# Kernel optimization log

Hardware: AMD Instinct MI355X
Metric: run time of the kernel (lower is better)

Reference implementation:

```python
import jax, jax.numpy as jnp
import numpy as np

N = 100000
E = 1600000
IN, HID, OUT = 128, 256, 128


def setup_inputs() -> dict:
    key = jax.random.key(0)
    ks = jax.random.split(key, 12)
    x = jax.random.normal(ks[0], (N, IN), dtype=jnp.float32)
    edge_index = jax.random.randint(ks[1], (2, E), 0, N, dtype=jnp.int64)
    def lin(k, fan_in, fan_out):
        bound = 1.0 / np.sqrt(fan_in)
        return jax.random.uniform(k, (fan_in, fan_out), jnp.float32, -bound, bound)
    return {
        "x": x,
        "edge_index": edge_index,
        # SAGEConv layer 1 (in -> hidden): Wl on aggregated neighbors (with bias), Wr on root
        "Wl1": lin(ks[2], IN, HID), "Wr1": lin(ks[3], IN, HID), "b1": jnp.zeros((HID,), jnp.float32),
        # SAGEConv layer 2 (hidden -> out)
        "Wl2": lin(ks[4], HID, OUT), "Wr2": lin(ks[5], HID, OUT), "b2": jnp.zeros((OUT,), jnp.float32),
        # classifier MLP: out -> hidden -> 2
        "Wc1": lin(ks[6], OUT, HID), "bc1": jnp.zeros((HID,), jnp.float32),
        "Wc2": lin(ks[7], HID, 2), "bc2": jnp.zeros((2,), jnp.float32),
    }


def _sage_conv(x, src, dst, Wl, Wr, b):
    # mean-aggregate neighbor features into dst, then lin_l(agg) + lin_r(x)
    agg = jax.ops.segment_sum(x[src], dst, num_segments=N)          # [N, d]
    cnt = jax.ops.segment_sum(jnp.ones((src.shape[0],), x.dtype), dst, num_segments=N)
    mean = agg / jnp.maximum(cnt, 1.0)[:, None]
    return mean @ Wl + x @ Wr + b


def reference(x, edge_index, Wl1, Wr1, b1, Wl2, Wr2, b2, Wc1, bc1, Wc2, bc2):
    src, dst = edge_index[0], edge_index[1]
    h = jax.nn.relu(_sage_conv(x, src, dst, Wl1, Wr1, b1))  # dropout = identity (eval)
    h = _sage_conv(h, src, dst, Wl2, Wr2, b2)               # node embeddings [N, OUT]
    logits = jax.nn.relu(h @ Wc1 + bc1) @ Wc2 + bc2          # [N, 2]
    return (h, logits)
```

## Files before the change

### kernel.cpp

```cpp
#include <hip/hip_runtime.h>

#define MAXDEG 64
#define BINSHIFT 10
#define CAP 20480
#define CHUNK 4096

typedef __bf16 bf16x8 __attribute__((ext_vector_type(8)));
typedef float f32x4 __attribute__((ext_vector_type(4)));

__device__ inline ushort f2bf(float f) {
    unsigned u = __builtin_bit_cast(unsigned, f);
    return (ushort)((u + 0x7fffu + ((u >> 16) & 1u)) >> 16);
}
__device__ inline float bf2f(ushort h) {
    unsigned u = ((unsigned)h) << 16;
    return __builtin_bit_cast(float, u);
}

__device__ inline void split8(const float* __restrict__ p, bf16x8& hi, bf16x8& lo) {
    float4 v0 = *(const float4*)p;
    float4 v1 = *(const float4*)(p + 4);
    float f[8] = {v0.x, v0.y, v0.z, v0.w, v1.x, v1.y, v1.z, v1.w};
    #pragma unroll
    for (int j = 0; j < 8; ++j) {
        __bf16 h = (__bf16)f[j];
        hi[j] = h;
        lo[j] = (__bf16)(f[j] - (float)h);
    }
}

__global__ __launch_bounds__(256) void bin_edges(
    const int* __restrict__ src, const int* __restrict__ dst,
    int* __restrict__ bincnt, uint2* __restrict__ binbuf, int E)
{
    __shared__ int hist[128];
    __shared__ int base[128];
    const int t = threadIdx.x;
    if (t < 128) hist[t] = 0;
    __syncthreads();

    const int e0 = blockIdx.x * CHUNK;
    int s[16], d[16], sl[16];
    #pragma unroll
    for (int j = 0; j < 16; ++j) {
        int e = e0 + j * 256 + t;
        if (e < E) {
            s[j]  = src[e];
            d[j]  = dst[e];
            sl[j] = atomicAdd(&hist[d[j] >> BINSHIFT], 1);
        } else {
            d[j] = -1;
        }
    }
    __syncthreads();
    if (t < 128 && hist[t] > 0) base[t] = atomicAdd(&bincnt[t], hist[t]);
    __syncthreads();
    #pragma unroll
    for (int j = 0; j < 16; ++j) {
        if (d[j] >= 0) {
            int b = d[j] >> BINSHIFT;
            int pos = base[b] + sl[j];
            if (pos < CAP)
                binbuf[(size_t)b * CAP + pos] = make_uint2((unsigned)s[j], (unsigned)d[j]);
        }
    }
}

__global__ __launch_bounds__(512) void fill_buckets(
    const int* __restrict__ bincnt, const uint2* __restrict__ binbuf,
    int* __restrict__ deg, int* __restrict__ col, int N)
{
    __shared__ int ldeg[1024];
    const int b = blockIdx.x;
    const int t = threadIdx.x;
    ldeg[t] = 0;
    ldeg[t + 512] = 0;
    __syncthreads();
    int cnt = bincnt[b];
    cnt = cnt < CAP ? cnt : CAP;
    const uint2* seg = binbuf + (size_t)b * CAP;
    for (int i = t; i < cnt; i += 512) {
        uint2 e = seg[i];
        int slot = atomicAdd(&ldeg[e.y & 1023], 1);
        if (slot < MAXDEG) col[(size_t)e.y * MAXDEG + slot] = (int)e.x;
    }
    __syncthreads();
    int nb = b << BINSHIFT;
    #pragma unroll
    for (int u = 0; u < 2; ++u) {
        int i = t + u * 512;
        int node = nb + i;
        if (node < N) deg[node] = ldeg[i];
    }
}

__global__ __launch_bounds__(256) void xtobf(
    const float* __restrict__ X, ushort* __restrict__ Xb, int n4)
{
    int i = blockIdx.x * 256 + threadIdx.x;
    if (i >= n4) return;
    float4 v = *(const float4*)(X + (size_t)i * 4);
    *(ushort4*)(Xb + (size_t)i * 4) =
        make_ushort4(f2bf(v.x), f2bf(v.y), f2bf(v.z), f2bf(v.w));
}

__global__ __launch_bounds__(256) void wsplit(
    const float* __restrict__ W, ushort* __restrict__ Thi, ushort* __restrict__ Tlo,
    int K, int N)
{
    int idx = blockIdx.x * 256 + threadIdx.x;
    if (idx >= K * N) return;
    int n = idx / K, k = idx % K;
    float v = W[(size_t)k * N + n];
    ushort h = f2bf(v);
    Thi[idx] = h;
    Tlo[idx] = f2bf(v - bf2f(h));
}

__global__ void make_bcat(const float* __restrict__ b2, float* __restrict__ bcat) {
    int t = threadIdx.x;
    bcat[t] = t < 128 ? 0.f : b2[t - 128];
}

__global__ __launch_bounds__(256) void init_logits(
    const float* __restrict__ bc2, float* __restrict__ out, int M)
{
    int n = blockIdx.x * 256 + threadIdx.x;
    if (n < M) *(float2*)(out + (size_t)n * 2) = make_float2(bc2[0], bc2[1]);
}

__global__ __launch_bounds__(256) void agg_mean_bf16(
    const ushort* __restrict__ Xb, const int* __restrict__ col,
    const int* __restrict__ deg, float* __restrict__ out, int N)
{
    int gw = (blockIdx.x * 256 + threadIdx.x) >> 6;
    if (gw >= N) return;
    int lane = threadIdx.x & 63;
    int d = deg[gw];
    int dc = d < MAXDEG ? d : MAXDEG;
    const int* cl = col + (size_t)gw * MAXDEG;
    float a0 = 0.f, a1 = 0.f;
    int i = 0;
    for (; i + 4 <= dc; i += 4) {
        int4 id4 = *(const int4*)(cl + i);
        ushort2 v0 = *(const ushort2*)(Xb + (size_t)id4.x * 128 + lane * 2);
        ushort2 v1 = *(const ushort2*)(Xb + (size_t)id4.y * 128 + lane * 2);
        ushort2 v2 = *(const ushort2*)(Xb + (size_t)id4.z * 128 + lane * 2);
        ushort2 v3 = *(const ushort2*)(Xb + (size_t)id4.w * 128 + lane * 2);
        a0 += (bf2f(v0.x) + bf2f(v1.x)) + (bf2f(v2.x) + bf2f(v3.x));
        a1 += (bf2f(v0.y) + bf2f(v1.y)) + (bf2f(v2.y) + bf2f(v3.y));
    }
    for (; i < dc; ++i) {
        ushort2 v = *(const ushort2*)(Xb + (size_t)cl[i] * 128 + lane * 2);
        a0 += bf2f(v.x); a1 += bf2f(v.y);
    }
    float inv = 1.0f / (float)(d > 1 ? d : 1);
    *(float2*)(out + (size_t)gw * 128 + lane * 2) = make_float2(a0 * inv, a1 * inv);
}

__global__ __launch_bounds__(256) void agg_finish(
    const ushort* __restrict__ t2b, const float* __restrict__ tcat2,
    const int* __restrict__ col, const int* __restrict__ deg,
    float* __restrict__ h2, int N)
{
    int gw = (blockIdx.x * 256 + threadIdx.x) >> 6;
    if (gw >= N) return;
    int lane = threadIdx.x & 63;
    int d = deg[gw];
    int dc = d < MAXDEG ? d : MAXDEG;
    const int* cl = col + (size_t)gw * MAXDEG;
    float a0 = 0.f, a1 = 0.f;
    int i = 0;
    for (; i + 4 <= dc; i += 4) {
        int4 id4 = *(const int4*)(cl + i);
        ushort2 v0 = *(const ushort2*)(t2b + (size_t)id4.x * 128 + lane * 2);
        ushort2 v1 = *(const ushort2*)(t2b + (size_t)id4.y * 128 + lane * 2);
        ushort2 v2 = *(const ushort2*)(t2b + (size_t)id4.z * 128 + lane * 2);
        ushort2 v3 = *(const ushort2*)(t2b + (size_t)id4.w * 128 + lane * 2);
        a0 += (bf2f(v0.x) + bf2f(v1.x)) + (bf2f(v2.x) + bf2f(v3.x));
        a1 += (bf2f(v0.y) + bf2f(v1.y)) + (bf2f(v2.y) + bf2f(v3.y));
    }
    for (; i < dc; ++i) {
        ushort2 v = *(const ushort2*)(t2b + (size_t)cl[i] * 128 + lane * 2);
        a0 += bf2f(v.x); a1 += bf2f(v.y);
    }
    float inv = 1.0f / (float)(d > 1 ? d : 1);
    float2 hp = *(const float2*)(tcat2 + (size_t)gw * 128 + lane * 2);
    *(float2*)(h2 + (size_t)gw * 128 + lane * 2) =
        make_float2(a0 * inv + hp.x, a1 * inv + hp.y);
}

template<int K, int NPH, int MODE>
__global__ __launch_bounds__(512, 4) void gemm_tile(
    const float* __restrict__ A1, const float* __restrict__ A2,
    const ushort* __restrict__ B1hi, const ushort* __restrict__ B1lo,
    const ushort* __restrict__ B2hi, const ushort* __restrict__ B2lo,
    const float* __restrict__ bias, const float* __restrict__ Wc2,
    float* __restrict__ outf, ushort* __restrict__ outt2, int M, int relu)
{
    __shared__ __align__(16) ushort Ah[128 * 40];
    __shared__ __align__(16) ushort Al[128 * 40];
    __shared__ __align__(16) ushort BhS[256 * 40];
    __shared__ __align__(16) ushort BlS[256 * 40];
    __shared__ float sw0[256], sw1[256];

    const int t = threadIdx.x;
    if constexpr (MODE == 1) {
        if (t < 256) {
            sw0[t] = Wc2[t * 2 + 0];
            sw1[t] = Wc2[t * 2 + 1];
        }
    }

    const int m0 = blockIdx.x * 128;
    const int l  = t & 63;
    const int wv = t >> 6;
    const int wr = (wv >> 1) * 32;
    const int wc = (wv & 1) * 128;
    const int lr = l & 15;
    const int kb = l >> 4;

    const int sra = t >> 2;
    const int sq  = t & 3;
    const int srb = t >> 1;
    const int sh  = t & 1;

    f32x4 acc[2][8] = {};

    #pragma unroll
    for (int ph = 0; ph < NPH; ++ph) {
        const float*  A  = ph ? A2 : A1;
        const ushort* Bh = ph ? B2hi : B1hi;
        const ushort* Bl = ph ? B2lo : B1lo;
        for (int k0 = 0; k0 < K; k0 += 32) {
            __syncthreads();
            {
                int rg = m0 + sra;
                rg = rg < M ? rg : M - 1;
                const float* p = A + (size_t)rg * K + k0 + sq * 8;
                bf16x8 h0, l0;
                split8(p, h0, l0);
                int base = sra * 40 + sq * 8;
                *(bf16x8*)&Ah[base] = h0;
                *(bf16x8*)&Al[base] = l0;
            }
            {
                const ushort* ph_ = Bh + (size_t)srb * K + k0 + sh * 16;
                const ushort* pl_ = Bl + (size_t)srb * K + k0 + sh * 16;
                int base = srb * 40 + sh * 16;
                *(uint4*)&BhS[base]     = *(const uint4*)ph_;
                *(uint4*)&BhS[base + 8] = *(const uint4*)(ph_ + 8);
                *(uint4*)&BlS[base]     = *(const uint4*)pl_;
                *(uint4*)&BlS[base + 8] = *(const uint4*)(pl_ + 8);
            }
            __syncthreads();
            bf16x8 ah[2], al_[2];
            #pragma unroll
            for (int mi = 0; mi < 2; ++mi) {
                int off = (wr + mi * 16 + lr) * 40 + kb * 8;
                ah[mi]  = *(const bf16x8*)&Ah[off];
                al_[mi] = *(const bf16x8*)&Al[off];
            }
            #pragma unroll
            for (int nj = 0; nj < 8; ++nj) {
                int off = (wc + nj * 16 + lr) * 40 + kb * 8;
                bf16x8 bh = *(const bf16x8*)&BhS[off];
                bf16x8 bl = *(const bf16x8*)&BlS[off];
                #pragma unroll
                for (int mi = 0; mi < 2; ++mi) {
                    acc[mi][nj] = __builtin_amdgcn_mfma_f32_16x16x32_bf16(ah[mi],  bh, acc[mi][nj], 0, 0, 0);
                    acc[mi][nj] = __builtin_amdgcn_mfma_f32_16x16x32_bf16(al_[mi], bh, acc[mi][nj], 0, 0, 0);
                    acc[mi][nj] = __builtin_amdgcn_mfma_f32_16x16x32_bf16(ah[mi],  bl, acc[mi][nj], 0, 0, 0);
                }
            }
        }
    }

    if constexpr (MODE != 1) {
        #pragma unroll
        for (int nj = 0; nj < 8; ++nj) {
            int colg = wc + nj * 16 + lr;
            float bv = bias[colg];
            #pragma unroll
            for (int mi = 0; mi < 2; ++mi) {
                #pragma unroll
                for (int reg = 0; reg < 4; ++reg) {
                    int rowg = m0 + wr + mi * 16 + kb * 4 + reg;
                    if (rowg >= M) continue;
                    float v = acc[mi][nj][reg] + bv;
                    if (relu) v = fmaxf(v, 0.f);
                    if constexpr (MODE == 0) {
                        outf[(size_t)rowg * 256 + colg] = v;
                    } else {
                        if (wc == 0) outt2[(size_t)rowg * 128 + colg] = f2bf(v);
                        else         outf[(size_t)rowg * 128 + colg - 128] = v;
                    }
                }
            }
        }
    } else {
        #pragma unroll
        for (int mi = 0; mi < 2; ++mi) {
            #pragma unroll
            for (int reg = 0; reg < 4; ++reg) {
                float s0 = 0.f, s1 = 0.f;
                #pragma unroll
                for (int nj = 0; nj < 8; ++nj) {
                    int colg = wc + nj * 16 + lr;
                    float v = fmaxf(acc[mi][nj][reg] + bias[colg], 0.f);
                    s0 += v * sw0[colg];
                    s1 += v * sw1[colg];
                }
                #pragma unroll
                for (int mk = 1; mk < 16; mk <<= 1) {
                    s0 += __shfl_xor(s0, mk);
                    s1 += __shfl_xor(s1, mk);
                }
                int rowg = m0 + wr + mi * 16 + kb * 4 + reg;
                if (lr == 0 && rowg < M) {
                    atomicAdd(&outf[(size_t)rowg * 2 + 0], s0);
                    atomicAdd(&outf[(size_t)rowg * 2 + 1], s1);
                }
            }
        }
    }
}

extern "C" void kernel_launch(void* const* d_in, const int* in_sizes, int n_in,
                              void* d_out, int out_size, void* d_ws, size_t ws_size,
                              hipStream_t stream)
{
    const float* x   = (const float*)d_in[0];
    const int*   ei  = (const int*)d_in[1];
    const float* Wl1 = (const float*)d_in[2];
    const float* Wr1 = (const float*)d_in[3];
    const float* b1  = (const float*)d_in[4];
    const float* Wl2 = (const float*)d_in[5];
    const float* Wr2 = (const float*)d_in[6];
    const float* b2  = (const float*)d_in[7];
    const float* Wc1 = (const float*)d_in[8];
    const float* bc1 = (const float*)d_in[9];
    const float* Wc2 = (const float*)d_in[10];
    const float* bc2 = (const float*)d_in[11];

    const int N = in_sizes[0] / 128;
    const int E = in_sizes[1] / 2;
    const int nbins = (N + (1 << BINSHIFT) - 1) >> BINSHIFT;

    char* ws = (char*)d_ws;
    size_t off = 0;
    auto alloc = [&](size_t bytes) -> void* {
        void* p = ws + off;
        off += (bytes + 255) & ~(size_t)255;
        return p;
    };
    const size_t NE128 = (size_t)N * 128;
    const size_t NE256 = (size_t)N * 256;

    int*    bincnt = (int*)alloc((size_t)nbins * 4);
    int*    deg  = (int*)alloc((size_t)N * 4);
    int*    colb = (int*)alloc((size_t)N * MAXDEG * 4);
    char*   bufA = (char*)alloc(NE256 * 4);
    char*   bufB = (char*)alloc(NE256 * 4);
    ushort* wl1h = (ushort*)alloc(256 * 128 * 2); ushort* wl1l = (ushort*)alloc(256 * 128 * 2);
    ushort* wr1h = (ushort*)alloc(256 * 128 * 2); ushort* wr1l = (ushort*)alloc(256 * 128 * 2);
    ushort* w2h  = (ushort*)alloc(256 * 256 * 2); ushort* w2l  = (ushort*)alloc(256 * 256 * 2);
    ushort* wc1h = (ushort*)alloc(256 * 128 * 2); ushort* wc1l = (ushort*)alloc(256 * 128 * 2);
    float*  bcat = (float*)alloc(256 * 4);

    uint2*  binbuf = (uint2*)bufA;
    float*  a1    = (float*)bufA;
    ushort* t2b   = (ushort*)bufA;
    float*  tcat2 = (float*)(bufA + NE128 * 2);
    ushort* xb    = (ushort*)bufB;
    float*  h1    = (float*)bufB;

    float* h2     = (float*)d_out;
    float* logits = (float*)d_out + NE128;

    const int gm = (N + 127) / 128;

    hipMemsetAsync(bincnt, 0, (size_t)nbins * 4, stream);

    bin_edges<<<dim3((E + CHUNK - 1) / CHUNK), dim3(256), 0, stream>>>(
        ei, ei + E, bincnt, binbuf, E);
    fill_buckets<<<dim3(nbins), dim3(512), 0, stream>>>(bincnt, binbuf, deg, colb, N);

    xtobf<<<dim3((int)(NE128 / 4 + 255) / 256), dim3(256), 0, stream>>>(x, xb, (int)(NE128 / 4));
    wsplit<<<dim3(128), dim3(256), 0, stream>>>(Wl1, wl1h, wl1l, 128, 256);
    wsplit<<<dim3(128), dim3(256), 0, stream>>>(Wr1, wr1h, wr1l, 128, 256);
    wsplit<<<dim3(128), dim3(256), 0, stream>>>(Wl2, w2h, w2l, 256, 128);
    wsplit<<<dim3(128), dim3(256), 0, stream>>>(Wr2, w2h + 128 * 256, w2l + 128 * 256, 256, 128);
    wsplit<<<dim3(128), dim3(256), 0, stream>>>(Wc1, wc1h, wc1l, 128, 256);
    make_bcat<<<dim3(1), dim3(256), 0, stream>>>(b2, bcat);
    init_logits<<<dim3((N + 255) / 256), dim3(256), 0, stream>>>(bc2, logits, N);

    agg_mean_bf16<<<dim3((N + 3) / 4), dim3(256), 0, stream>>>(xb, colb, deg, a1, N);
    gemm_tile<128, 2, 0><<<dim3(gm), dim3(512), 0, stream>>>(
        a1, x, wl1h, wl1l, wr1h, wr1l, b1, nullptr, h1, nullptr, N, 1);

    gemm_tile<256, 1, 3><<<dim3(gm), dim3(512), 0, stream>>>(
        h1, nullptr, w2h, w2l, nullptr, nullptr, bcat, nullptr, tcat2, t2b, N, 0);

    agg_finish<<<dim3((N + 3) / 4), dim3(256), 0, stream>>>(
        t2b, tcat2, colb, deg, h2, N);

    gemm_tile<128, 1, 1><<<dim3(gm), dim3(512), 0, stream>>>(
        h2, nullptr, wc1h, wc1l, nullptr, nullptr, bc1, Wc2, logits, nullptr, N, 1);
}
```

Before: 428.0 us.

## Split GEMM columns across a 2D grid and widen gather loads to 8 bytes

The GEMM kernel now tiles the output 128 columns per block with a second grid dimension, so each block does half the N-width. This halves the accumulator and LDS footprint per block, which should raise occupancy and give more blocks, but the A tile, including its hi/lo split, is now loaded and converted twice. The aggregation kernels split each 64-lane wave into two half-waves that take alternate neighbour groups with 8-byte loads, then combine through a cross-lane shuffle. That doubles the number of gathers in flight per wave.

```diff
diff --git a/kernel.cpp b/kernel.cpp
--- a/kernel.cpp
+++ b/kernel.cpp
@@ -136,26 +136,38 @@
     int gw = (blockIdx.x * 256 + threadIdx.x) >> 6;
     if (gw >= N) return;
     int lane = threadIdx.x & 63;
+    int sub = lane >> 5;
+    int c4  = (lane & 31) * 4;
     int d = deg[gw];
     int dc = d < MAXDEG ? d : MAXDEG;
     const int* cl = col + (size_t)gw * MAXDEG;
-    float a0 = 0.f, a1 = 0.f;
+    float a0 = 0.f, a1 = 0.f, a2 = 0.f, a3 = 0.f;
     int i = 0;
-    for (; i + 4 <= dc; i += 4) {
-        int4 id4 = *(const int4*)(cl + i);
-        ushort2 v0 = *(const ushort2*)(Xb + (size_t)id4.x * 128 + lane * 2);
-        ushort2 v1 = *(const ushort2*)(Xb + (size_t)id4.y * 128 + lane * 2);
-        ushort2 v2 = *(const ushort2*)(Xb + (size_t)id4.z * 128 + lane * 2);
-        ushort2 v3 = *(const ushort2*)(Xb + (size_t)id4.w * 128 + lane * 2);
+    for (; i + 8 <= dc; i += 8) {
+        int4 id = *(const int4*)(cl + i + sub * 4);
+        ushort4 v0 = *(const ushort4*)(Xb + (size_t)id.x * 128 + c4);
+        ushort4 v1 = *(const ushort4*)(Xb + (size_t)id.y * 128 + c4);
+        ushort4 v2 = *(const ushort4*)(Xb + (size_t)id.z * 128 + c4);
+        ushort4 v3 = *(const ushort4*)(Xb + (size_t)id.w * 128 + c4);
         a0 += (bf2f(v0.x) + bf2f(v1.x)) + (bf2f(v2.x) + bf2f(v3.x));
         a1 += (bf2f(v0.y) + bf2f(v1.y)) + (bf2f(v2.y) + bf2f(v3.y));
-    }
-    for (; i < dc; ++i) {
-        ushort2 v = *(const ushort2*)(Xb + (size_t)cl[i] * 128 + lane * 2);
-        a0 += bf2f(v.x); a1 += bf2f(v.y);
-    }
-    float inv = 1.0f / (float)(d > 1 ? d : 1);
-    *(float2*)(out + (size_t)gw * 128 + lane * 2) = make_float2(a0 * inv, a1 * inv);
+        a2 += (bf2f(v0.z) + bf2f(v1.z)) + (bf2f(v2.z) + bf2f(v3.z));
+        a3 += (bf2f(v0.w) + bf2f(v1.w)) + (bf2f(v2.w) + bf2f(v3.w));
+    }
+    for (; i < dc; i += 2) {
+        int j = i + sub;
+        if (j < dc) {
+            ushort4 v = *(const ushort4*)(Xb + (size_t)cl[j] * 128 + c4);
+            a0 += bf2f(v.x); a1 += bf2f(v.y); a2 += bf2f(v.z); a3 += bf2f(v.w);
+        }
+    }
+    a0 += __shfl_xor(a0, 32); a1 += __shfl_xor(a1, 32);
+    a2 += __shfl_xor(a2, 32); a3 += __shfl_xor(a3, 32);
+    if (sub == 0) {
+        float inv = 1.0f / (float)(d > 1 ? d : 1);
+        *(float4*)(out + (size_t)gw * 128 + c4) =
+            make_float4(a0 * inv, a1 * inv, a2 * inv, a3 * inv);
+    }
 }
 
 __global__ __launch_bounds__(256) void agg_finish(
@@ -166,28 +178,39 @@
     int gw = (blockIdx.x * 256 + threadIdx.x) >> 6;
     if (gw >= N) return;
     int lane = threadIdx.x & 63;
+    int sub = lane >> 5;
+    int c4  = (lane & 31) * 4;
     int d = deg[gw];
     int dc = d < MAXDEG ? d : MAXDEG;
     const int* cl = col + (size_t)gw * MAXDEG;
-    float a0 = 0.f, a1 = 0.f;
+    float a0 = 0.f, a1 = 0.f, a2 = 0.f, a3 = 0.f;
     int i = 0;
-    for (; i + 4 <= dc; i += 4) {
-        int4 id4 = *(const int4*)(cl + i);
-        ushort2 v0 = *(const ushort2*)(t2b + (size_t)id4.x * 128 + lane * 2);
-        ushort2 v1 = *(const ushort2*)(t2b + (size_t)id4.y * 128 + lane * 2);
-        ushort2 v2 = *(const ushort2*)(t2b + (size_t)id4.z * 128 + lane * 2);
-        ushort2 v3 = *(const ushort2*)(t2b + (size_t)id4.w * 128 + lane * 2);
+    for (; i + 8 <= dc; i += 8) {
+        int4 id = *(const int4*)(cl + i + sub * 4);
+        ushort4 v0 = *(const ushort4*)(t2b + (size_t)id.x * 128 + c4);
+        ushort4 v1 = *(const ushort4*)(t2b + (size_t)id.y * 128 + c4);
+        ushort4 v2 = *(const ushort4*)(t2b + (size_t)id.z * 128 + c4);
+        ushort4 v3 = *(const ushort4*)(t2b + (size_t)id.w * 128 + c4);
         a0 += (bf2f(v0.x) + bf2f(v1.x)) + (bf2f(v2.x) + bf2f(v3.x));
         a1 += (bf2f(v0.y) + bf2f(v1.y)) + (bf2f(v2.y) + bf2f(v3.y));
-    }
-    for (; i < dc; ++i) {
-        ushort2 v = *(const ushort2*)(t2b + (size_t)cl[i] * 128 + lane * 2);
-        a0 += bf2f(v.x); a1 += bf2f(v.y);
-    }
-    float inv = 1.0f / (float)(d > 1 ? d : 1);
-    float2 hp = *(const float2*)(tcat2 + (size_t)gw * 128 + lane * 2);
-    *(float2*)(h2 + (size_t)gw * 128 + lane * 2) =
-        make_float2(a0 * inv + hp.x, a1 * inv + hp.y);
+        a2 += (bf2f(v0.z) + bf2f(v1.z)) + (bf2f(v2.z) + bf2f(v3.z));
+        a3 += (bf2f(v0.w) + bf2f(v1.w)) + (bf2f(v2.w) + bf2f(v3.w));
+    }
+    for (; i < dc; i += 2) {
+        int j = i + sub;
+        if (j < dc) {
+            ushort4 v = *(const ushort4*)(t2b + (size_t)cl[j] * 128 + c4);
+            a0 += bf2f(v.x); a1 += bf2f(v.y); a2 += bf2f(v.z); a3 += bf2f(v.w);
+        }
+    }
+    a0 += __shfl_xor(a0, 32); a1 += __shfl_xor(a1, 32);
+    a2 += __shfl_xor(a2, 32); a3 += __shfl_xor(a3, 32);
+    if (sub == 0) {
+        float inv = 1.0f / (float)(d > 1 ? d : 1);
+        float4 hp = *(const float4*)(tcat2 + (size_t)gw * 128 + c4);
+        *(float4*)(h2 + (size_t)gw * 128 + c4) = make_float4(
+            a0 * inv + hp.x, a1 * inv + hp.y, a2 * inv + hp.z, a3 * inv + hp.w);
+    }
 }
 
 template<int K, int NPH, int MODE>
@@ -200,9 +223,9 @@
 {
     __shared__ __align__(16) ushort Ah[128 * 40];
     __shared__ __align__(16) ushort Al[128 * 40];
-    __shared__ __align__(16) ushort BhS[256 * 40];
-    __shared__ __align__(16) ushort BlS[256 * 40];
-    __shared__ float sw0[256], sw1[256];
+    __shared__ __align__(16) ushort BhS[128 * 40];
+    __shared__ __align__(16) ushort BlS[128 * 40];
+    __shared__ float sw0[MODE == 1 ? 256 : 4], sw1[MODE == 1 ? 256 : 4];
 
     const int t = threadIdx.x;
     if constexpr (MODE == 1) {
@@ -213,19 +236,18 @@
     }
 
     const int m0 = blockIdx.x * 128;
+    const int n0 = blockIdx.y * 128;
     const int l  = t & 63;
     const int wv = t >> 6;
     const int wr = (wv >> 1) * 32;
-    const int wc = (wv & 1) * 128;
+    const int wc = (wv & 1) * 64;
     const int lr = l & 15;
     const int kb = l >> 4;
 
-    const int sra = t >> 2;
-    const int sq  = t & 3;
-    const int srb = t >> 1;
-    const int sh  = t & 1;
-
-    f32x4 acc[2][8] = {};
+    const int sr = t >> 2;
+    const int sq = t & 3;
+
+    f32x4 acc[2][4] = {};
 
     #pragma unroll
     for (int ph = 0; ph < NPH; ++ph) {
@@ -235,23 +257,21 @@
         for (int k0 = 0; k0 < K; k0 += 32) {
             __syncthreads();
             {
-                int rg = m0 + sra;
+                int rg = m0 + sr;
                 rg = rg < M ? rg : M - 1;
                 const float* p = A + (size_t)rg * K + k0 + sq * 8;
                 bf16x8 h0, l0;
                 split8(p, h0, l0);
-                int base = sra * 40 + sq * 8;
+                int base = sr * 40 + sq * 8;
                 *(bf16x8*)&Ah[base] = h0;
                 *(bf16x8*)&Al[base] = l0;
             }
             {
-                const ushort* ph_ = Bh + (size_t)srb * K + k0 + sh * 16;
-                const ushort* pl_ = Bl + (size_t)srb * K + k0 + sh * 16;
-                int base = srb * 40 + sh * 16;
-                *(uint4*)&BhS[base]     = *(const uint4*)ph_;
-                *(uint4*)&BhS[base + 8] = *(const uint4*)(ph_ + 8);
-                *(uint4*)&BlS[base]     = *(const uint4*)pl_;
-                *(uint4*)&BlS[base + 8] = *(const uint4*)(pl_ + 8);
+                const ushort* ph_ = Bh + (size_t)(n0 + sr) * K + k0 + sq * 8;
+                const ushort* pl_ = Bl + (size_t)(n0 + sr) * K + k0 + sq * 8;
+                int base = sr * 40 + sq * 8;
+                *(uint4*)&BhS[base] = *(const uint4*)ph_;
+                *(uint4*)&BlS[base] = *(const uint4*)pl_;
             }
             __syncthreads();
             bf16x8 ah[2], al_[2];
@@ -262,7 +282,7 @@
                 al_[mi] = *(const bf16x8*)&Al[off];
             }
             #pragma unroll
-            for (int nj = 0; nj < 8; ++nj) {
+            for (int nj = 0; nj < 4; ++nj) {
                 int off = (wc + nj * 16 + lr) * 40 + kb * 8;
                 bf16x8 bh = *(const bf16x8*)&BhS[off];
                 bf16x8 bl = *(const bf16x8*)&BlS[off];
@@ -278,8 +298,9 @@
 
     if constexpr (MODE != 1) {
         #pragma unroll
-        for (int nj = 0; nj < 8; ++nj) {
-            int colg = wc + nj * 16 + lr;
+        for (int nj = 0; nj < 4; ++nj) {
+            int lc   = wc + nj * 16 + lr;
+            int colg = n0 + lc;
             float bv = bias[colg];
             #pragma unroll
             for (int mi = 0; mi < 2; ++mi) {
@@ -292,8 +313,8 @@
                     if constexpr (MODE == 0) {
                         outf[(size_t)rowg * 256 + colg] = v;
                     } else {
-                        if (wc == 0) outt2[(size_t)rowg * 128 + colg] = f2bf(v);
-                        else         outf[(size_t)rowg * 128 + colg - 128] = v;
+                        if (n0 == 0) outt2[(size_t)rowg * 128 + lc] = f2bf(v);
+                        else         outf[(size_t)rowg * 128 + lc] = v;
                     }
                 }
             }
@@ -305,8 +326,8 @@
             for (int reg = 0; reg < 4; ++reg) {
                 float s0 = 0.f, s1 = 0.f;
                 #pragma unroll
-                for (int nj = 0; nj < 8; ++nj) {
-                    int colg = wc + nj * 16 + lr;
+                for (int nj = 0; nj < 4; ++nj) {
+                    int colg = n0 + wc + nj * 16 + lr;
                     float v = fmaxf(acc[mi][nj][reg] + bias[colg], 0.f);
                     s0 += v * sw0[colg];
                     s1 += v * sw1[colg];
@@ -396,15 +417,15 @@
     init_logits<<<dim3((N + 255) / 256), dim3(256), 0, stream>>>(bc2, logits, N);
 
     agg_mean_bf16<<<dim3((N + 3) / 4), dim3(256), 0, stream>>>(xb, colb, deg, a1, N);
-    gemm_tile<128, 2, 0><<<dim3(gm), dim3(512), 0, stream>>>(
+    gemm_tile<128, 2, 0><<<dim3(gm, 2), dim3(512), 0, stream>>>(
         a1, x, wl1h, wl1l, wr1h, wr1l, b1, nullptr, h1, nullptr, N, 1);
 
-    gemm_tile<256, 1, 3><<<dim3(gm), dim3(512), 0, stream>>>(
+    gemm_tile<256, 1, 3><<<dim3(gm, 2), dim3(512), 0, stream>>>(
         h1, nullptr, w2h, w2l, nullptr, nullptr, bcat, nullptr, tcat2, t2b, N, 0);
 
     agg_finish<<<dim3((N + 3) / 4), dim3(256), 0, stream>>>(
         t2b, tcat2, colb, deg, h2, N);
 
-    gemm_tile<128, 1, 1><<<dim3(gm), dim3(512), 0, stream>>>(
+    gemm_tile<128, 1, 1><<<dim3(gm, 2), dim3(512), 0, stream>>>(
         h2, nullptr, wc1h, wc1l, nullptr, nullptr, bc1, Wc2, logits, nullptr, N, 1);
 }
```

New measurement: 407.6 us. -4.8%, faster.
